# Kernel optimization log

Hardware: AMD Instinct MI355X
Metric: run time of the kernel (lower is better)

The kernel has to match this reference:

```python
import jax, jax.numpy as jnp
import numpy as np

V = 32000; D = 1024; L = 2; H = 16; KVH = 4; HD = D // H; E = 8; FF = 2048; K = 2
B = 2; S = 1024; WINDOW = 4096; THETA = 10000.0; EPS = 1e-6


def setup_inputs() -> dict:
    key = jax.random.key(0)
    ks = jax.random.split(key, 12)
    std = 0.02
    return {
        'tokens': jax.random.randint(ks[0], (B, S), 0, V),
        'tok_emb': jax.random.normal(ks[1], (V, D), jnp.float32),  # nn.Embedding default N(0,1)
        'norm1_w': jnp.ones((L, D), jnp.float32),
        'norm2_w': jnp.ones((L, D), jnp.float32),
        'wq': jax.random.normal(ks[2], (L, D, D), jnp.float32) * std,
        'wk': jax.random.normal(ks[3], (L, KVH * HD, D), jnp.float32) * std,
        'wv': jax.random.normal(ks[4], (L, KVH * HD, D), jnp.float32) * std,
        'wo': jax.random.normal(ks[5], (L, D, D), jnp.float32) * std,
        'router_w': jax.random.normal(ks[6], (L, E, D), jnp.float32) * (std / np.sqrt(D)),
        'w1': jax.random.normal(ks[7], (L, E, FF, D), jnp.float32) * std,
        'w2': jax.random.normal(ks[8], (L, E, FF, D), jnp.float32) * std,
        'w3': jax.random.normal(ks[9], (L, E, D, FF), jnp.float32) * std,
        'normf_w': jnp.ones((D,), jnp.float32),
        'head_w': jax.random.normal(ks[10], (V, D), jnp.float32) * std,
    }


def rmsnorm(x, w):
    # F.normalize(x, dim=-1, eps) * w * sqrt(d)
    n = jnp.linalg.norm(x, axis=-1, keepdims=True)
    return x / jnp.maximum(n, EPS) * w * np.float32(np.sqrt(x.shape[-1]))


def rope(x, cos, sin):
    # x: (b, s, h, hd); pairs are interleaved (even, odd) per view_as_complex
    x2 = x.reshape(x.shape[:-1] + (-1, 2))
    x0, x1 = x2[..., 0], x2[..., 1]
    o0 = x0 * cos - x1 * sin
    o1 = x0 * sin + x1 * cos
    return jnp.stack([o0, o1], axis=-1).reshape(x.shape)


def attention(x, wq, wk, wv, wo, cos, sin):
    b, s, _ = x.shape
    q = (x @ wq.T).reshape(b, s, H, HD)
    k = (x @ wk.T).reshape(b, s, KVH, HD)
    v = (x @ wv.T).reshape(b, s, KVH, HD)
    q = rope(q, cos, sin)
    k = rope(k, cos, sin)
    g = H // KVH
    k = jnp.repeat(k, g, axis=2)
    v = jnp.repeat(v, g, axis=2)
    scores = jnp.einsum('bqhd,bkhd->bhqk', q, k) / np.float32(np.sqrt(HD))
    i = jnp.arange(s)[:, None]; j = jnp.arange(s)[None, :]
    allow = (j <= i) & (i - j < WINDOW)  # causal + sliding window
    scores = jnp.where(allow, scores, -jnp.inf)
    attn = jax.nn.softmax(scores, axis=-1)
    out = jnp.einsum('bhqk,bkhd->bqhd', attn, v).reshape(b, s, D)
    return out @ wo.T


def moe(x, router_w, w1, w2, w3):
    b, s, d = x.shape
    logits = jnp.einsum('bsd,ed->bse', x, router_w)
    probs = jax.nn.softmax(logits, axis=-1)
    _, idx = jax.lax.top_k(probs, K)                      # (b, s, K)
    mask = jax.nn.one_hot(idx, E, dtype=x.dtype).sum(-2)  # (b, s, E) binary
    xt = x.reshape(-1, d)           # (T, d)
    mt = mask.reshape(-1, E)        # (T, E)
    # Dense masked dispatch: every expert computed on all tokens, combine masks to zero
    u = jnp.einsum('td,efd->etf', xt, w1)
    g = jax.nn.silu(u) * jnp.einsum('td,efd->etf', xt, w2)
    y = jnp.einsum('etf,edf->etd', g, w3)
    out = jnp.einsum('etd,te->td', y, mt).reshape(b, s, d)  # unweighted combine (per source)
    # aux losses
    z_loss = jnp.mean(jax.scipy.special.logsumexp(logits, axis=-1)) ** 2
    load = probs.sum(axis=0)  # (s, E), matching probs.sum(dim=0) in source
    load_loss = (jnp.std(load, ddof=1) / jnp.mean(load)) ** 2
    aux = 0.001 * z_loss + 0.001 * load_loss
    return out, aux


def _rope_tables(dtype):
    freqs = 1.0 / (THETA ** (np.arange(0, HD, 2, dtype=np.float32) / HD))
    ang = np.arange(S, dtype=np.float32)[:, None] * freqs[None, :]
    cos = jnp.asarray(np.cos(ang), dtype)[None, :, None, :]
    sin = jnp.asarray(np.sin(ang), dtype)[None, :, None, :]
    return cos, sin


def reference(tokens, tok_emb, norm1_w, norm2_w, wq, wk, wv, wo, router_w, w1, w2, w3, normf_w, head_w):
    x = tok_emb[tokens]  # (B, S, D)
    cos, sin = _rope_tables(x.dtype)
    attn_scale = np.float32(1.0 / np.sqrt(2.0 * L))
    aux_total = jnp.zeros((), x.dtype)
    for l in range(L):
        x = x + attn_scale * attention(rmsnorm(x, norm1_w[l]), wq[l], wk[l], wv[l], wo[l], cos, sin)
        mo, aux = moe(rmsnorm(x, norm2_w[l]), router_w[l], w1[l], w2[l], w3[l])
        x = x + mo
        aux_total = aux_total + aux
    logits = rmsnorm(x, normf_w) @ head_w.T
    return logits, aux_total
```

## Files before the change

kernel.cpp:

```cpp
#include <hip/hip_runtime.h>
#include <math.h>

#define DEV __device__ __forceinline__

using v8s = __attribute__((ext_vector_type(8))) short;
using v4f = __attribute__((ext_vector_type(4))) float;

DEV short f2bf(float f) {
    unsigned u = __float_as_uint(f);
    unsigned r = (u + 0x7fffu + ((u >> 16) & 1u)) >> 16;
    return (short)(unsigned short)r;
}
DEV float bf2f(short s) {
    return __uint_as_float(((unsigned)(unsigned short)s) << 16);
}

DEV void gload16(const short* g, short* l) {
    __builtin_amdgcn_global_load_lds((const __attribute__((address_space(1))) void*)g,
                                     (__attribute__((address_space(3))) void*)l,
                                     16, 0, 0);
}

DEV void raw_barrier() { asm volatile("s_barrier" ::: "memory"); }

DEV float block_sum256(float v, float* red) {
    __syncthreads();
#pragma unroll
    for (int o = 32; o >= 1; o >>= 1) v += __shfl_down(v, o, 64);
    if ((threadIdx.x & 63) == 0) red[threadIdx.x >> 6] = v;
    __syncthreads();
    return red[0] + red[1] + red[2] + red[3];
}
DEV float block_max256(float v, float* red) {
    __syncthreads();
#pragma unroll
    for (int o = 32; o >= 1; o >>= 1) v = fmaxf(v, __shfl_down(v, o, 64));
    if ((threadIdx.x & 63) == 0) red[threadIdx.x >> 6] = v;
    __syncthreads();
    return fmaxf(fmaxf(red[0], red[1]), fmaxf(red[2], red[3]));
}


__global__ __launch_bounds__(256) void conv_tile(const float* __restrict__ src,
                                                 short* __restrict__ hi, short* __restrict__ lo,
                                                 long nGroups, int Kg, long chunkRows, long chunkPanelStride) {
    const long panelElems = 128L * Kg * 8;
    for (long idx = (long)blockIdx.x * 256 + threadIdx.x; idx < nGroups; idx += (long)gridDim.x * 256) {
        long rrow = idx / Kg; int g = (int)(idx - rrow * Kg);
        long c = rrow / chunkRows; int ri = (int)(rrow - c * chunkRows);
        long panel = c * chunkPanelStride + (ri >> 7);
        long dst = panel * panelElems + ((long)(g >> 2) << 12) + ((long)(g & 3) << 10) + ((long)(ri & 127) << 3);
        const float4 f0 = ((const float4*)src)[idx * 2];
        const float4 f1 = ((const float4*)src)[idx * 2 + 1];
        short h0 = f2bf(f0.x), h1 = f2bf(f0.y), h2 = f2bf(f0.z), h3 = f2bf(f0.w);
        short h4 = f2bf(f1.x), h5 = f2bf(f1.y), h6 = f2bf(f1.z), h7 = f2bf(f1.w);
        *(ushort4*)(hi + dst)     = make_ushort4((unsigned short)h0, (unsigned short)h1,
                                                 (unsigned short)h2, (unsigned short)h3);
        *(ushort4*)(hi + dst + 4) = make_ushort4((unsigned short)h4, (unsigned short)h5,
                                                 (unsigned short)h6, (unsigned short)h7);
        if (lo) {
            short l0 = f2bf(f0.x - bf2f(h0)), l1 = f2bf(f0.y - bf2f(h1));
            short l2 = f2bf(f0.z - bf2f(h2)), l3 = f2bf(f0.w - bf2f(h3));
            short l4 = f2bf(f1.x - bf2f(h4)), l5 = f2bf(f1.y - bf2f(h5));
            short l6 = f2bf(f1.z - bf2f(h6)), l7 = f2bf(f1.w - bf2f(h7));
            *(ushort4*)(lo + dst)     = make_ushort4((unsigned short)l0, (unsigned short)l1,
                                                     (unsigned short)l2, (unsigned short)l3);
            *(ushort4*)(lo + dst + 4) = make_ushort4((unsigned short)l4, (unsigned short)l5,
                                                     (unsigned short)l6, (unsigned short)l7);
        }
    }
}

struct GemmP {
    const short* Ah; const short* Al;
    const short* Bh; const short* Bl;
    float* C; short* Ch; short* Cl;
    const int* cnt; const int* ppd; const int* lrow;
    long aPanelsZ;
    long strideAz;
    long strideBz, strideCz;
    int M, N, K, lda, ldc;
    float alpha;
    int outMode;
    int gqaB;
    int grouped;
    int causalSkip;
    int causalK;
    int ntiles, S, G;
};

template<bool SPLIT>
__global__ __launch_bounds__(256) void gemm_bt128(GemmP p) {
    const int lid = blockIdx.x;
    const int xcd = lid & 7, sI = lid >> 3;
    const int gi = xcd + 8 * (sI / p.S);
    if (gi >= p.G) return;
    const int mt = sI % p.S;
    const int nt = gi % p.ntiles;
    const int z  = gi / p.ntiles;
    if (p.causalSkip && nt > mt) return;

    const int tid = threadIdx.x;
    int Mz = p.grouped ? p.cnt[z] : p.M;
    if (mt * 128 >= Mz) return;

    long bOff;
    if (p.gqaB) { int b = z >> 4, h = z & 15; bOff = (long)(b * 4 + (h >> 2)) * p.strideBz; }
    else bOff = (long)z * p.strideBz;

    extern __shared__ short s0[];
    const int BUF = SPLIT ? 16384 : 8192;

    const int lane = tid & 63, w = tid >> 6;
    const int lr = lane & 15, lg = lane >> 4;
    const int wr = w >> 1, wc = w & 1;

    v4f acc[4][4];
#pragma unroll
    for (int i = 0; i < 4; ++i)
#pragma unroll
        for (int j = 0; j < 4; ++j) { acc[i][j][0] = 0.f; acc[i][j][1] = 0.f; acc[i][j][2] = 0.f; acc[i][j][3] = 0.f; }

    const short* bks  = p.Bh + bOff + (long)nt * 128 * p.K + (long)w * 1024 + lane * 8;
    const short* bksL = SPLIT ? p.Bl + bOff + (long)nt * 128 * p.K + (long)w * 1024 + lane * 8 : nullptr;

    long aPanel = (p.grouped ? (long)(p.ppd[z] >> 7) : (long)z * p.aPanelsZ) + mt;
    const short* aks  = p.Ah + aPanel * 128L * p.K + (long)w * 1024 + lane * 8;
    const short* aksL = SPLIT ? p.Al + aPanel * 128L * p.K + (long)w * 1024 + lane * 8 : nullptr;

    const int nIter = p.K >> 5;
    const int wb = w * 1024;
    {
        gload16(aks,       s0 + wb);
        gload16(aks + 512, s0 + wb + 512);
        gload16(bks,       s0 + 4096 + wb);
        gload16(bks + 512, s0 + 4096 + wb + 512);
        if (SPLIT) {
            gload16(aksL,       s0 + 8192 + wb);
            gload16(aksL + 512, s0 + 8192 + wb + 512);
            gload16(bksL,       s0 + 12288 + wb);
            gload16(bksL + 512, s0 + 12288 + wb + 512);
        }
    }
    for (int i = 0; i < nIter; ++i) {
        const int cur = i & 1;
        if (i + 1 < nIter) {
            raw_barrier();
            const long kb = (long)(i + 1) * 4096;
            short* base = s0 + (cur ^ 1) * BUF;
            gload16(aks + kb,       base + wb);
            gload16(aks + kb + 512, base + wb + 512);
            gload16(bks + kb,       base + 4096 + wb);
            gload16(bks + kb + 512, base + 4096 + wb + 512);
            if (SPLIT) {
                gload16(aksL + kb,       base + 8192 + wb);
                gload16(aksL + kb + 512, base + 8192 + wb + 512);
                gload16(bksL + kb,       base + 12288 + wb);
                gload16(bksL + kb + 512, base + 12288 + wb + 512);
            }
            if constexpr (SPLIT) asm volatile("s_waitcnt vmcnt(8)" ::: "memory");
            else                 asm volatile("s_waitcnt vmcnt(4)" ::: "memory");
        } else {
            asm volatile("s_waitcnt vmcnt(0)" ::: "memory");
        }
        raw_barrier();
        const short* base = s0 + cur * BUF;
        const int abase = lg * 1024 + (wr * 64 + lr) * 8;
        const int bbase = 4096 + lg * 1024 + (wc * 64 + lr) * 8;
        v8s ah[4], bh[4];
#pragma unroll
        for (int q = 0; q < 4; ++q) {
            ah[q] = *(const v8s*)(base + abase + q * 128);
            bh[q] = *(const v8s*)(base + bbase + q * 128);
        }
        if constexpr (SPLIT) {
            v8s al[4], bl[4];
#pragma unroll
            for (int q = 0; q < 4; ++q) {
                al[q] = *(const v8s*)(base + 8192 + abase + q * 128);
                bl[q] = *(const v8s*)(base + 8192 + bbase + q * 128);
            }
#pragma unroll
            for (int mi = 0; mi < 4; ++mi)
#pragma unroll
                for (int nj = 0; nj < 4; ++nj) {
                    acc[mi][nj] = __builtin_amdgcn_mfma_f32_16x16x32_bf16(ah[mi], bh[nj], acc[mi][nj], 0, 0, 0);
                    acc[mi][nj] = __builtin_amdgcn_mfma_f32_16x16x32_bf16(al[mi], bh[nj], acc[mi][nj], 0, 0, 0);
                    acc[mi][nj] = __builtin_amdgcn_mfma_f32_16x16x32_bf16(ah[mi], bl[nj], acc[mi][nj], 0, 0, 0);
                }
        } else {
#pragma unroll
            for (int mi = 0; mi < 4; ++mi)
#pragma unroll
                for (int nj = 0; nj < 4; ++nj)
                    acc[mi][nj] = __builtin_amdgcn_mfma_f32_16x16x32_bf16(ah[mi], bh[nj], acc[mi][nj], 0, 0, 0);
        }
    }

#pragma unroll
    for (int mi = 0; mi < 4; ++mi) {
        const int mrow = mt * 128 + wr * 64 + mi * 16 + lg * 4;
#pragma unroll
        for (int nj = 0; nj < 4; ++nj) {
            const int ncol = nt * 128 + wc * 64 + nj * 16 + lr;
            if (ncol < p.N) {
#pragma unroll
                for (int rr = 0; rr < 4; ++rr) {
                    const int m = mrow + rr;
                    if (m < Mz) {
                        float v = acc[mi][nj][rr] * p.alpha;
                        long crow;
                        if (p.grouped == 1)      crow = p.ppd[z] + m;
                        else if (p.grouped == 2) crow = p.lrow[z * 2048 + m];
                        else                     crow = m;
                        long co = (long)z * p.strideCz + crow * (long)p.ldc + ncol;
                        if (p.outMode == 0) p.C[co] = v;
                        else                p.C[co] += v;
                    }
                }
            }
        }
    }
}

template<bool SPLIT>
__global__ __launch_bounds__(512) void gemm_bt256(GemmP p) {
    const int lid = blockIdx.x;
    const int xcd = lid & 7, sI = lid >> 3;
    const int gi = xcd + 8 * (sI / p.S);
    if (gi >= p.G) return;
    const int mt = sI % p.S;
    const int nt = gi % p.ntiles;
    const int z  = gi / p.ntiles;
    if (p.causalSkip && nt > 2 * mt + 1) return;

    const int tid = threadIdx.x;
    int Mz = p.grouped ? p.cnt[z] : p.M;
    if (mt * 256 >= Mz) return;

    long bOff;
    if (p.gqaB) { int b = z >> 4, h = z & 15; bOff = (long)(b * 4 + (h >> 2)) * p.strideBz; }
    else bOff = (long)z * p.strideBz;

    extern __shared__ short s0[];
    const int BUF = SPLIT ? 24576 : 12288;

    const int lane = tid & 63, w = tid >> 6;
    const int lr = lane & 15, lg = lane >> 4;
    const int wr = w >> 1, wc = w & 1;

    v4f acc[4][4];
#pragma unroll
    for (int i = 0; i < 4; ++i)
#pragma unroll
        for (int j = 0; j < 4; ++j) { acc[i][j][0] = 0.f; acc[i][j][1] = 0.f; acc[i][j][2] = 0.f; acc[i][j][3] = 0.f; }

    const short* bks  = p.Bh + bOff + (long)nt * 128 * p.K + (long)w * 512 + lane * 8;
    const short* bksL = SPLIT ? p.Bl + bOff + (long)nt * 128 * p.K + (long)w * 512 + lane * 8 : nullptr;
    const long aPanelBase = (p.grouped ? (long)(p.ppd[z] >> 7) : (long)z * p.aPanelsZ) + 2L * mt;
    const int u0 = 2 * w, u1 = 2 * w + 1;
    const short* aks0  = p.Ah + (aPanelBase + (u0 >> 3)) * 128L * p.K + (long)(u0 & 7) * 512 + lane * 8;
    const short* aks1  = p.Ah + (aPanelBase + (u1 >> 3)) * 128L * p.K + (long)(u1 & 7) * 512 + lane * 8;
    const short* aks0L = SPLIT ? p.Al + (aPanelBase + (u0 >> 3)) * 128L * p.K + (long)(u0 & 7) * 512 + lane * 8 : nullptr;
    const short* aks1L = SPLIT ? p.Al + (aPanelBase + (u1 >> 3)) * 128L * p.K + (long)(u1 & 7) * 512 + lane * 8 : nullptr;
    short* dA0 = s0 + u0 * 512;
    short* dA1 = s0 + u1 * 512;
    short* dB  = s0 + 8192 + w * 512;

    const int nIter = p.K >> 5;
    {
        gload16(aks0, dA0);
        gload16(aks1, dA1);
        gload16(bks,  dB);
        if (SPLIT) {
            gload16(aks0L, dA0 + 12288);
            gload16(aks1L, dA1 + 12288);
            gload16(bksL,  dB + 12288);
        }
    }
    for (int i = 0; i < nIter; ++i) {
        const int cur = i & 1;
        if (i + 1 < nIter) {
            raw_barrier();
            const long kb = (long)(i + 1) * 4096;
            const int boff = (cur ^ 1) * BUF;
            gload16(aks0 + kb, dA0 + boff);
            gload16(aks1 + kb, dA1 + boff);
            gload16(bks + kb,  dB + boff);
            if (SPLIT) {
                gload16(aks0L + kb, dA0 + boff + 12288);
                gload16(aks1L + kb, dA1 + boff + 12288);
                gload16(bksL + kb,  dB + boff + 12288);
            }
            if constexpr (SPLIT) asm volatile("s_waitcnt vmcnt(6)" ::: "memory");
            else                 asm volatile("s_waitcnt vmcnt(3)" ::: "memory");
        } else {
            asm volatile("s_waitcnt vmcnt(0)" ::: "memory");
        }
        raw_barrier();
        const short* base = s0 + cur * BUF;
        const int abase = (wr >> 1) * 4096 + lg * 1024 + ((wr & 1) * 64 + lr) * 8;
        const int bbase = 8192 + lg * 1024 + (wc * 64 + lr) * 8;
        v8s ah[4], bh[4];
#pragma unroll
        for (int q = 0; q < 4; ++q) {
            ah[q] = *(const v8s*)(base + abase + q * 128);
            bh[q] = *(const v8s*)(base + bbase + q * 128);
        }
        if constexpr (SPLIT) {
            v8s al[4], bl[4];
#pragma unroll
            for (int q = 0; q < 4; ++q) {
                al[q] = *(const v8s*)(base + 12288 + abase + q * 128);
                bl[q] = *(const v8s*)(base + 12288 + bbase + q * 128);
            }
#pragma unroll
            for (int mi = 0; mi < 4; ++mi)
#pragma unroll
                for (int nj = 0; nj < 4; ++nj) {
                    acc[mi][nj] = __builtin_amdgcn_mfma_f32_16x16x32_bf16(ah[mi], bh[nj], acc[mi][nj], 0, 0, 0);
                    acc[mi][nj] = __builtin_amdgcn_mfma_f32_16x16x32_bf16(al[mi], bh[nj], acc[mi][nj], 0, 0, 0);
                    acc[mi][nj] = __builtin_amdgcn_mfma_f32_16x16x32_bf16(ah[mi], bl[nj], acc[mi][nj], 0, 0, 0);
                }
        } else {
#pragma unroll
            for (int mi = 0; mi < 4; ++mi)
#pragma unroll
                for (int nj = 0; nj < 4; ++nj)
                    acc[mi][nj] = __builtin_amdgcn_mfma_f32_16x16x32_bf16(ah[mi], bh[nj], acc[mi][nj], 0, 0, 0);
        }
    }

#pragma unroll
    for (int mi = 0; mi < 4; ++mi) {
        const int mrow = mt * 256 + wr * 64 + mi * 16 + lg * 4;
#pragma unroll
        for (int nj = 0; nj < 4; ++nj) {
            const int ncol = nt * 128 + wc * 64 + nj * 16 + lr;
            if (ncol < p.N) {
#pragma unroll
                for (int rr = 0; rr < 4; ++rr) {
                    const int m = mrow + rr;
                    if (m < Mz) {
                        float v = acc[mi][nj][rr] * p.alpha;
                        long crow;
                        if (p.grouped == 1)      crow = p.ppd[z] + m;
                        else if (p.grouped == 2) crow = p.lrow[z * 2048 + m];
                        else                     crow = m;
                        long co = (long)z * p.strideCz + crow * (long)p.ldc + ncol;
                        if (p.outMode == 0) p.C[co] = v;
                        else                p.C[co] += v;
                    }
                }
            }
        }
    }
}

__global__ __launch_bounds__(256) void gemm_pv(GemmP p) {
    const int lid = blockIdx.x;
    const int xcd = lid & 7, sI = lid >> 3;
    const int gi = xcd + 8 * (sI / p.S);
    if (gi >= p.G) return;
    const int mt = sI % p.S;
    const int z  = gi;
    const int tid = threadIdx.x;

    const int b = z >> 4, h = z & 15;
    const long bOff = (long)(b * 4 + (h >> 2)) * p.strideBz;

    extern __shared__ short s0[];
    short* Ahs = s0;
    short* Bhs = s0 + 4096;
    short* Als = s0 + 8192;
    short* Bls = s0 + 12288;

    const int lane = tid & 63, w = tid >> 6;
    const int lr = lane & 15, lg = lane >> 4;
    const int wr = w >> 1, wc = w & 1;

    v4f acc[4][4];
#pragma unroll
    for (int i = 0; i < 4; ++i)
#pragma unroll
        for (int j = 0; j < 4; ++j) { acc[i][j][0] = 0.f; acc[i][j][1] = 0.f; acc[i][j][2] = 0.f; acc[i][j][3] = 0.f; }

    const short* bks  = p.Bh + bOff + (long)w * 1024 + lane * 8;
    const short* bksL = p.Bl + bOff + (long)w * 1024 + lane * 8;

    const int r = tid & 127;
    const int kgA = tid >> 7;
    const int am = mt * 128 + r;
    const long arowoff = (long)z * p.strideAz + (long)am * p.lda;
    const short* aH = p.Ah + arowoff + kgA * 16;
    const short* aL = p.Al + arowoff + kgA * 16;
    short* sA0 = s0 + (kgA * 256 + r) * 8; short* sA1 = sA0 + 1024;
    short* sA0l = s0 + 8192 + (kgA * 256 + r) * 8; short* sA1l = sA0l + 1024;

    const int kEnd = min(p.K, (mt + 1) * 128);
    const int wb = w * 1024;
    for (int k0 = 0; k0 < kEnd; k0 += 32) {
        const long kb = (long)k0 * 128;
        uint4 a0 = *(const uint4*)(aH + k0);
        uint4 a1 = *(const uint4*)(aH + k0 + 8);
        uint4 a0l = *(const uint4*)(aL + k0);
        uint4 a1l = *(const uint4*)(aL + k0 + 8);
        __syncthreads();
        gload16(bks + kb,       Bhs + wb);
        gload16(bks + kb + 512, Bhs + wb + 512);
        gload16(bksL + kb,       Bls + wb);
        gload16(bksL + kb + 512, Bls + wb + 512);
        *(uint4*)sA0 = a0; *(uint4*)sA1 = a1;
        *(uint4*)sA0l = a0l; *(uint4*)sA1l = a1l;
        __syncthreads();
        const int abase = lg * 1024 + (wr * 64 + lr) * 8;
        const int bbase = lg * 1024 + (wc * 64 + lr) * 8;
        v8s ah[4], bh[4], al[4], bl[4];
#pragma unroll
        for (int q = 0; q < 4; ++q) {
            ah[q] = *(const v8s*)(Ahs + abase + q * 128);
            bh[q] = *(const v8s*)(Bhs + bbase + q * 128);
            al[q] = *(const v8s*)(Als + abase + q * 128);
            bl[q] = *(const v8s*)(Bls + bbase + q * 128);
        }
#pragma unroll
        for (int mi = 0; mi < 4; ++mi)
#pragma unroll
            for (int nj = 0; nj < 4; ++nj) {
                acc[mi][nj] = __builtin_amdgcn_mfma_f32_16x16x32_bf16(ah[mi], bh[nj], acc[mi][nj], 0, 0, 0);
                acc[mi][nj] = __builtin_amdgcn_mfma_f32_16x16x32_bf16(al[mi], bh[nj], acc[mi][nj], 0, 0, 0);
                acc[mi][nj] = __builtin_amdgcn_mfma_f32_16x16x32_bf16(ah[mi], bl[nj], acc[mi][nj], 0, 0, 0);
            }
    }

#pragma unroll
    for (int mi = 0; mi < 4; ++mi) {
        const int mrow = mt * 128 + wr * 64 + mi * 16 + lg * 4;
#pragma unroll
        for (int nj = 0; nj < 4; ++nj) {
            const int ncol = wc * 64 + nj * 16 + lr;
            if (ncol < 64) {
#pragma unroll
                for (int rr = 0; rr < 4; ++rr) {
                    const int m = mrow + rr;
                    float v = acc[mi][nj][rr];
                    int grow = b * 1024 + m, col = h * 64 + ncol;
                    long dst = ((long)(grow >> 7)) * 131072 + ((long)(col >> 5) << 12)
                             + ((long)((col >> 3) & 3) << 10) + ((long)(grow & 127) << 3) + (col & 7);
                    short hi = f2bf(v);
                    p.Ch[dst] = hi;
                    p.Cl[dst] = f2bf(v - bf2f(hi));
                }
            }
        }
    }
}

__global__ __launch_bounds__(256) void embed_kernel(const int* toks, const float* emb, float* X) {
    const int t = blockIdx.x;
    const int tok = toks[t];
    const float4* s = (const float4*)(emb + (size_t)tok * 1024);
    float4* d = (float4*)(X + (size_t)t * 1024);
    d[threadIdx.x] = s[threadIdx.x];
}

__global__ __launch_bounds__(256) void rmsnorm_split(const float* X, const float* w, short* oh, short* ol) {
    __shared__ float red[4];
    const long t = blockIdx.x;
    const float* r = X + t * 1024;
    float ss = 0.f;
    for (int j = threadIdx.x; j < 1024; j += 256) { float f = r[j]; ss += f * f; }
    ss = block_sum256(ss, red);
    const float sc = 32.f / fmaxf(sqrtf(ss), 1e-6f);
    if (threadIdx.x < 128) {
        const int g = threadIdx.x, f = g * 8;
        float v[8];
#pragma unroll
        for (int j = 0; j < 8; ++j) v[j] = r[f + j] * sc * w[f + j];
        long dst = (t >> 7) * 131072 + ((long)(g >> 2) << 12) + ((long)(g & 3) << 10) + ((t & 127) << 3);
        short h[8], lo[8];
#pragma unroll
        for (int j = 0; j < 8; ++j) { h[j] = f2bf(v[j]); lo[j] = f2bf(v[j] - bf2f(h[j])); }
        *(ushort4*)(oh + dst)     = make_ushort4((unsigned short)h[0], (unsigned short)h[1], (unsigned short)h[2], (unsigned short)h[3]);
        *(ushort4*)(oh + dst + 4) = make_ushort4((unsigned short)h[4], (unsigned short)h[5], (unsigned short)h[6], (unsigned short)h[7]);
        *(ushort4*)(ol + dst)     = make_ushort4((unsigned short)lo[0], (unsigned short)lo[1], (unsigned short)lo[2], (unsigned short)lo[3]);
        *(ushort4*)(ol + dst + 4) = make_ushort4((unsigned short)lo[4], (unsigned short)lo[5], (unsigned short)lo[6], (unsigned short)lo[7]);
    }
}

struct RopeF { float f[32]; };

__global__ __launch_bounds__(256) void rope_q_kernel(const float* QKV, short* OH, short* OL, RopeF rf) {
    const int idx = blockIdx.x * 256 + threadIdx.x;
    const int pp = idx & 31, h = (idx >> 5) & 15, s = (idx >> 9) & 1023, b = idx >> 19;
    const float* src = QKV + ((size_t)(b * 1024 + s)) * 1536 + h * 64 + 2 * pp;
    const float x0 = src[0], x1 = src[1];
    const float ang = (float)s * rf.f[pp];
    float sn, cs; sincosf(ang, &sn, &cs);
    const float o0 = x0 * cs - x1 * sn, o1 = x0 * sn + x1 * cs;
    const int z = b * 16 + h, d = 2 * pp;
    const long off = (long)z * 65536 + (long)(s >> 7) * 8192
                   + ((long)(d >> 5) << 12) + ((long)((d >> 3) & 3) << 10)
                   + ((long)(s & 127) << 3) + (d & 7);
    short h0 = f2bf(o0); OH[off] = h0; OL[off] = f2bf(o0 - bf2f(h0));
    short h1 = f2bf(o1); OH[off + 1] = h1; OL[off + 1] = f2bf(o1 - bf2f(h1));
}

__global__ __launch_bounds__(256) void rope_k_kernel(const float* QKV, short* KH, short* KL, RopeF rf) {
    const int idx = blockIdx.x * 256 + threadIdx.x;
    const int pp = idx & 31, kv = (idx >> 5) & 3, s = (idx >> 7) & 1023, b = idx >> 17;
    const float* src = QKV + ((size_t)(b * 1024 + s)) * 1536 + 1024 + kv * 64 + 2 * pp;
    const float x0 = src[0], x1 = src[1];
    const float ang = (float)s * rf.f[pp];
    float sn, cs; sincosf(ang, &sn, &cs);
    const float o0 = x0 * cs - x1 * sn, o1 = x0 * sn + x1 * cs;
    const int z = b * 4 + kv, d = 2 * pp;
    const long off = (long)z * 65536 + (long)(s >> 7) * 8192
                   + ((long)(d >> 5) << 12) + ((long)((d >> 3) & 3) << 10)
                   + ((long)(s & 127) << 3) + (d & 7);
    short h0 = f2bf(o0); KH[off] = h0; KL[off] = f2bf(o0 - bf2f(h0));
    short h1 = f2bf(o1); KH[off + 1] = h1; KL[off + 1] = f2bf(o1 - bf2f(h1));
}

__global__ __launch_bounds__(256) void transpose_v_kernel(const float* QKV, short* VH, short* VL) {
    const int idx = blockIdx.x * 256 + threadIdx.x;
    const int d = idx & 63, kv = (idx >> 6) & 3, s = (idx >> 8) & 1023, b = idx >> 18;
    const float f = QKV[((size_t)(b * 1024 + s)) * 1536 + 1280 + kv * 64 + d];
    const int z = b * 4 + kv;
    const long off = (long)z * 131072 + ((long)(s >> 5) << 12) + ((long)((s >> 3) & 3) << 10)
                   + ((long)d << 3) + (s & 7);
    short hi = f2bf(f);
    VH[off] = hi; VL[off] = f2bf(f - bf2f(hi));
    VH[off + 512] = 0; VL[off + 512] = 0;
}

__global__ __launch_bounds__(256) void attn_softmax(float* SC) {
    const long row = blockIdx.x;
    const int i = (int)(row & 1023);
    float* r = SC + row * 1024;
    __shared__ float buf[1024];
    __shared__ float red[4];
    const int n = i + 1;
    for (int j = threadIdx.x; j < n; j += 256) buf[j] = r[j];
    __syncthreads();
    float m = -INFINITY;
    for (int j = threadIdx.x; j < n; j += 256) m = fmaxf(m, buf[j]);
    m = block_max256(m, red);
    float s = 0.f;
    for (int j = threadIdx.x; j < n; j += 256) { float e = expf(buf[j] - m); buf[j] = e; s += e; }
    s = block_sum256(s, red);
    const float inv = 1.f / s;
    short* rh = (short*)r;
    short* rl = rh + 1024;
    __syncthreads();
    for (int j = threadIdx.x; j < 1024; j += 256) {
        float pv = (j < n) ? buf[j] * inv : 0.f;
        short hi = f2bf(pv);
        rh[j] = hi;
        rl[j] = f2bf(pv - bf2f(hi));
    }
}

__global__ __launch_bounds__(256) void router_kernel(const float* X, const float* wn, const float* rw,
                                                     float* probs, float* lse, int* cnt, int* ltok, int* lrow) {
    __shared__ float xs[1024];
    __shared__ float red[4];
    __shared__ float lg[8];
    const int t = blockIdx.x;
    const float* r = X + (size_t)t * 1024;
    for (int j = threadIdx.x; j < 1024; j += 256) xs[j] = r[j];
    __syncthreads();
    float ss = 0.f;
    for (int j = threadIdx.x; j < 1024; j += 256) ss += xs[j] * xs[j];
    ss = block_sum256(ss, red);
    const float sc = 32.f / fmaxf(sqrtf(ss), 1e-6f);
    float acc[8] = {0, 0, 0, 0, 0, 0, 0, 0};
    for (int j = threadIdx.x; j < 1024; j += 256) {
        const float xv = xs[j] * wn[j];
#pragma unroll
        for (int e = 0; e < 8; ++e) acc[e] += xv * rw[e * 1024 + j];
    }
#pragma unroll
    for (int e = 0; e < 8; ++e) {
        float s = block_sum256(acc[e], red);
        if (threadIdx.x == 0) lg[e] = s * sc;
    }
    __syncthreads();
    if (threadIdx.x == 0) {
        float m = lg[0];
        for (int e = 1; e < 8; ++e) m = fmaxf(m, lg[e]);
        float ex[8], se = 0.f;
        for (int e = 0; e < 8; ++e) { ex[e] = expf(lg[e] - m); se += ex[e]; }
        const float inv = 1.f / se;
        float pr[8];
        for (int e = 0; e < 8; ++e) { pr[e] = ex[e] * inv; probs[(size_t)t * 8 + e] = pr[e]; }
        lse[t] = m + logf(se);
        int i1 = 0;
        for (int e = 1; e < 8; ++e) if (pr[e] > pr[i1]) i1 = e;
        int i2 = (i1 == 0) ? 1 : 0;
        for (int e = 0; e < 8; ++e) if (e != i1 && pr[e] > pr[i2]) i2 = e;
        int s1 = atomicAdd(&cnt[i1], 1); ltok[i1 * 2048 + s1] = t; lrow[i1 * 2048 + s1] = 2 * t;
        int s2 = atomicAdd(&cnt[i2], 1); ltok[i2 * 2048 + s2] = t; lrow[i2 * 2048 + s2] = 2 * t + 1;
    }
}

__global__ void prefix_kernel(const int* cnt, int* ppd) {
    if (threadIdx.x == 0 && blockIdx.x == 0) {
        int a = 0;
        for (int e = 0; e < 8; ++e) { ppd[e] = a; a += ((cnt[e] + 255) >> 8) << 8; }
    }
}

__global__ __launch_bounds__(256) void gather_kernel(const short* XNH, const short* XNL,
                                                     const int* cnt, const int* ppd, const int* ltok,
                                                     short* GXNH, short* GXNL) {
    const int e = blockIdx.y, i = blockIdx.x;
    if (i >= cnt[e]) return;
    const int t = ltok[e * 2048 + i];
    const int pd = ppd[e] + i;
    const int plane = threadIdx.x >> 7, g = threadIdx.x & 127;
    const long goff = ((long)(g >> 2) << 12) + ((long)(g & 3) << 10);
    const long src = (long)(t >> 7) * 131072 + goff + ((t & 127) << 3);
    const long dst = (long)(pd >> 7) * 131072 + goff + ((pd & 127) << 3);
    const short* S = plane ? XNL : XNH;
    short* D = plane ? GXNL : GXNH;
    *(uint4*)(D + dst) = *(const uint4*)(S + src);
}

__global__ __launch_bounds__(256) void silu_mul(const float* U, short* HH, short* HL) {
    const int row = blockIdx.x, g = threadIdx.x;
    const float* ur = U + (long)row * 4096 + g * 8;
    const float4 u0 = *(const float4*)ur, u1 = *(const float4*)(ur + 4);
    const float4 g0 = *(const float4*)(ur + 2048), g1 = *(const float4*)(ur + 2052);
    float h[8];
    h[0] = (u0.x / (1.f + expf(-u0.x))) * g0.x;
    h[1] = (u0.y / (1.f + expf(-u0.y))) * g0.y;
    h[2] = (u0.z / (1.f + expf(-u0.z))) * g0.z;
    h[3] = (u0.w / (1.f + expf(-u0.w))) * g0.w;
    h[4] = (u1.x / (1.f + expf(-u1.x))) * g1.x;
    h[5] = (u1.y / (1.f + expf(-u1.y))) * g1.y;
    h[6] = (u1.z / (1.f + expf(-u1.z))) * g1.z;
    h[7] = (u1.w / (1.f + expf(-u1.w))) * g1.w;
    const long dst = (long)(row >> 7) * 262144 + ((long)(g >> 2) << 12) + ((long)(g & 3) << 10) + ((row & 127) << 3);
    short hh[8], ll[8];
#pragma unroll
    for (int j = 0; j < 8; ++j) { hh[j] = f2bf(h[j]); ll[j] = f2bf(h[j] - bf2f(hh[j])); }
    *(ushort4*)(HH + dst)     = make_ushort4((unsigned short)hh[0], (unsigned short)hh[1], (unsigned short)hh[2], (unsigned short)hh[3]);
    *(ushort4*)(HH + dst + 4) = make_ushort4((unsigned short)hh[4], (unsigned short)hh[5], (unsigned short)hh[6], (unsigned short)hh[7]);
    *(ushort4*)(HL + dst)     = make_ushort4((unsigned short)ll[0], (unsigned short)ll[1], (unsigned short)ll[2], (unsigned short)ll[3]);
    *(ushort4*)(HL + dst + 4) = make_ushort4((unsigned short)ll[4], (unsigned short)ll[5], (unsigned short)ll[6], (unsigned short)ll[7]);
}

__global__ __launch_bounds__(256) void combine_kernel(float* X, const float* Y) {
    const int i4 = blockIdx.x * 256 + threadIdx.x;
    const int t = i4 >> 8, d4 = i4 & 255;
    float4 x = ((float4*)X)[i4];
    const float4 a = ((const float4*)Y)[(size_t)(2 * t) * 256 + d4];
    const float4 b = ((const float4*)Y)[(size_t)(2 * t + 1) * 256 + d4];
    x.x += a.x + b.x; x.y += a.y + b.y; x.z += a.z + b.z; x.w += a.w + b.w;
    ((float4*)X)[i4] = x;
}

__global__ __launch_bounds__(256) void aux_kernel(const float* probs, const float* lse, float* auxb, int layer) {
    __shared__ float red[4];
    float sl = 0.f;
    for (int t = threadIdx.x; t < 2048; t += 256) sl += lse[t];
    sl = block_sum256(sl, red);
    float s1 = 0.f, s2 = 0.f;
    for (int i = threadIdx.x; i < 8192; i += 256) {
        const float l = probs[i] + probs[8192 + i];
        s1 += l; s2 += l * l;
    }
    s1 = block_sum256(s1, red);
    s2 = block_sum256(s2, red);
    if (threadIdx.x == 0) {
        const float ml = sl / 2048.f;
        const float mean = s1 / 8192.f;
        const float var = fmaxf((s2 - s1 * s1 / 8192.f) / 8191.f, 0.f);
        auxb[layer] = 0.001f * (ml * ml + var / (mean * mean));
    }
}

__global__ void finalize_aux(const float* auxb, float* out) {
    if (threadIdx.x == 0 && blockIdx.x == 0)
        out[(size_t)2 * 1024 * 32000] = auxb[0] + auxb[1];
}

static void run_gemm128(hipStream_t s, bool split, GemmP& p, int ntiles, int mtiles, int zdim) {
    p.ntiles = ntiles; p.S = mtiles;
    p.G = ntiles * zdim;
    int Gp = (p.G + 7) & ~7;
    long nb = (long)Gp * mtiles;
    dim3 g((unsigned)nb, 1, 1), b(256);
    if (split) gemm_bt128<true><<<g, b, 65536, s>>>(p);
    else       gemm_bt128<false><<<g, b, 32768, s>>>(p);
}

static void run_gemm256(hipStream_t s, bool split, GemmP& p, int ntiles, int mtiles, int zdim) {
    p.ntiles = ntiles; p.S = mtiles;
    p.G = ntiles * zdim;
    int Gp = (p.G + 7) & ~7;
    long nb = (long)Gp * mtiles;
    dim3 g((unsigned)nb, 1, 1), b(512);
    if (split) gemm_bt256<true><<<g, b, 98304, s>>>(p);
    else       gemm_bt256<false><<<g, b, 49152, s>>>(p);
}

static void run_tile(hipStream_t s, const float* src, short* hi, short* lo,
                     long rows, int K, long chunkRows, long chunkPanelStride) {
    long groups = rows * (K / 8);
    long nb = (groups + 255) / 256; if (nb > 2048) nb = 2048;
    conv_tile<<<(unsigned)nb, 256, 0, s>>>(src, hi, lo, groups, K / 8, chunkRows, chunkPanelStride);
}

extern "C" void kernel_launch(void* const* d_in, const int* in_sizes, int n_in,
                              void* d_out, int out_size, void* d_ws, size_t ws_size,
                              hipStream_t stream) {
    (void)in_sizes; (void)n_in; (void)out_size; (void)ws_size;
    const int*   tokens = (const int*)d_in[0];
    const float* tok_emb = (const float*)d_in[1];
    const float* norm1 = (const float*)d_in[2];
    const float* norm2 = (const float*)d_in[3];
    const float* wq = (const float*)d_in[4];
    const float* wk = (const float*)d_in[5];
    const float* wv = (const float*)d_in[6];
    const float* wo = (const float*)d_in[7];
    const float* rw = (const float*)d_in[8];
    const float* w1 = (const float*)d_in[9];
    const float* w2 = (const float*)d_in[10];
    const float* w3 = (const float*)d_in[11];
    const float* normf = (const float*)d_in[12];
    const float* headw = (const float*)d_in[13];
    float* out = (float*)d_out;

    char* w = (char*)d_ws;
    const size_t MB = 1024ull * 1024ull;
    float* X    = (float*)(w + 0);
    short* XNH  = (short*)(w + 8 * MB);
    short* XNL  = (short*)(w + 12 * MB);
    short* QRH  = (short*)(w + 16 * MB);
    short* QRL  = (short*)(w + 20 * MB);
    short* AOH  = QRH;
    short* AOL  = QRL;
    short* KRH  = (short*)(w + 24 * MB);
    short* KRL  = (short*)(w + 25 * MB);
    short* VTH  = (short*)(w + 26 * MB);
    short* VTL  = (short*)(w + 28 * MB);
    float* QKV  = (float*)(w + 32 * MB);
    float* SC   = (float*)(w + 32 * MB);
    short* GXNH = (short*)(w + 32 * MB);
    short* GXNL = (short*)(w + 44 * MB);
    float* U    = (float*)(w + 56 * MB);
    short* HH   = (short*)(w + 152 * MB);
    short* HL   = (short*)(w + 176 * MB);
    float* Y    = (float*)(w + 200 * MB);
    float* PROBS= (float*)(w + 216 * MB);
    float* LSE  = (float*)(w + 216 * MB + 65536);
    int*   CNT  = (int*)  (w + 216 * MB + 73728);
    int*   PPD  = (int*)  (w + 216 * MB + 73856);
    int*   LTOK = (int*)  (w + 216 * MB + 74240);
    int*   LROW = (int*)  (w + 216 * MB + 74240 + 65536);
    float* AUXB = (float*)(w + 216 * MB + 74240 + 131072);
    short* WQKVH = (short*)(w + 218 * MB);
    short* WQKVL = (short*)(w + 224 * MB);
    short* WOH   = (short*)(w + 230 * MB);
    short* WOL   = (short*)(w + 234 * MB);
    short* W12H  = (short*)(w + 238 * MB);
    short* W12L  = (short*)(w + 302 * MB);
    short* W3H   = (short*)(w + 366 * MB);
    short* W3L   = (short*)(w + 398 * MB);
    short* HDH   = (short*)(w + 302 * MB);

    RopeF rf;
    for (int i = 0; i < 32; ++i) {
        float t = (float)pow(10000.0, (double)(2 * i) / 64.0);
        rf.f[i] = 1.0f / t;
    }

    for (int l = 0; l < 2; ++l) {
        long qo = (long)l * 1572864;
        run_tile(stream, wq + (long)l * 1048576, WQKVH + qo,           WQKVL + qo,           1024, 1024, 1024, 8);
        run_tile(stream, wk + (long)l * 262144,  WQKVH + qo + 1048576, WQKVL + qo + 1048576, 256, 1024, 256, 2);
        run_tile(stream, wv + (long)l * 262144,  WQKVH + qo + 1310720, WQKVL + qo + 1310720, 256, 1024, 256, 2);
    }
    run_tile(stream, wo, WOH, WOL, 2048, 1024, 2048, 16);

    embed_kernel<<<2048, 256, 0, stream>>>(tokens, tok_emb, X);

    for (int l = 0; l < 2; ++l) {
        const bool msp = (l == 0);
        run_tile(stream, w1 + (long)l * 16777216, W12H,           msp ? W12L : nullptr,           16384, 1024, 2048, 32);
        run_tile(stream, w2 + (long)l * 16777216, W12H + 2097152, msp ? W12L + 2097152 : nullptr, 16384, 1024, 2048, 32);
        run_tile(stream, w3 + (long)l * 16777216, W3H,            msp ? W3L : nullptr,            8192, 2048, 8192, 64);

        rmsnorm_split<<<2048, 256, 0, stream>>>(X, norm1 + l * 1024, XNH, XNL);

        { GemmP p = {}; p.Ah = XNH; p.Al = XNL; p.Bh = WQKVH + (long)l * 1572864; p.Bl = WQKVL + (long)l * 1572864;
          p.C = QKV; p.M = 2048; p.N = 1536; p.K = 1024; p.aPanelsZ = 16; p.ldc = 1536; p.alpha = 1.f;
          run_gemm128(stream, true, p, 12, 16, 1); }

        rope_q_kernel<<<4096, 256, 0, stream>>>(QKV, QRH, QRL, rf);
        rope_k_kernel<<<1024, 256, 0, stream>>>(QKV, KRH, KRL, rf);
        transpose_v_kernel<<<2048, 256, 0, stream>>>(QKV, VTH, VTL);

        { GemmP p = {}; p.Ah = QRH; p.Al = QRL; p.Bh = KRH; p.Bl = KRL; p.C = SC;
          p.M = 1024; p.N = 1024; p.K = 64; p.aPanelsZ = 8; p.ldc = 1024;
          p.strideBz = 65536; p.strideCz = 1048576;
          p.alpha = 0.125f; p.gqaB = 1; p.causalSkip = 1;
          run_gemm256(stream, true, p, 8, 4, 32); }

        attn_softmax<<<32768, 256, 0, stream>>>(SC);

        { GemmP p = {}; p.Ah = (short*)SC; p.Al = (short*)SC + 1024; p.Bh = VTH; p.Bl = VTL; p.Ch = AOH; p.Cl = AOL;
          p.M = 1024; p.N = 64; p.K = 1024; p.lda = 2048;
          p.strideAz = 2097152; p.strideBz = 131072;
          p.ntiles = 1; p.S = 8; p.G = 32;
          long nb = 32L * 8;
          gemm_pv<<<dim3((unsigned)nb), dim3(256), 32768, stream>>>(p); }

        { GemmP p = {}; p.Ah = AOH; p.Al = AOL; p.Bh = WOH + (long)l * 1048576; p.Bl = WOL + (long)l * 1048576; p.C = X;
          p.M = 2048; p.N = 1024; p.K = 1024; p.aPanelsZ = 16; p.ldc = 1024;
          p.alpha = 0.5f; p.outMode = 1;
          run_gemm128(stream, true, p, 8, 16, 1); }

        rmsnorm_split<<<2048, 256, 0, stream>>>(X, norm2 + l * 1024, XNH, XNL);
        hipMemsetAsync(CNT, 0, 8 * sizeof(int), stream);
        router_kernel<<<2048, 256, 0, stream>>>(X, norm2 + l * 1024, rw + (size_t)l * 8 * 1024,
                                                PROBS, LSE, CNT, LTOK, LROW);
        prefix_kernel<<<1, 64, 0, stream>>>(CNT, PPD);
        { dim3 gg(2048, 8); gather_kernel<<<gg, 256, 0, stream>>>(XNH, XNL, CNT, PPD, LTOK, GXNH, GXNL); }

        { GemmP p = {}; p.Ah = GXNH; p.Al = GXNL; p.Bh = W12H; p.Bl = W12L; p.C = U;
          p.M = 2048; p.N = 4096; p.K = 1024; p.ldc = 4096;
          p.strideBz = 4194304; p.strideCz = 0; p.alpha = 1.f; p.grouped = 1;
          p.cnt = CNT; p.ppd = PPD; p.lrow = LROW;
          run_gemm256(stream, msp, p, 32, 8, 8); }
        silu_mul<<<6144, 256, 0, stream>>>(U, HH, HL);
        { GemmP p = {}; p.Ah = HH; p.Al = HL; p.Bh = W3H; p.Bl = W3L; p.C = Y;
          p.M = 2048; p.N = 1024; p.K = 2048; p.ldc = 1024;
          p.strideBz = 2097152; p.strideCz = 0; p.alpha = 1.f; p.grouped = 2;
          p.cnt = CNT; p.ppd = PPD; p.lrow = LROW;
          run_gemm256(stream, msp, p, 8, 8, 8); }
        combine_kernel<<<2048, 256, 0, stream>>>(X, Y);
        aux_kernel<<<1, 256, 0, stream>>>(PROBS, LSE, AUXB, l);

        if (l == 0)
            run_tile(stream, headw, HDH, nullptr, 32000, 1024, 32000, 250);
    }

    rmsnorm_split<<<2048, 256, 0, stream>>>(X, normf, XNH, XNL);
    { GemmP p = {}; p.Ah = XNH; p.Bh = HDH; p.C = out;
      p.M = 2048; p.N = 32000; p.K = 1024; p.aPanelsZ = 16; p.ldc = 32000; p.alpha = 1.f;
      run_gemm256(stream, false, p, 250, 8, 1); }
    finalize_aux<<<1, 1, 0, stream>>>(AUXB, out);
}
```

Before: 2.164 ms.

## Reorder GEMM block mapping, fuse rope/transpose kernels, use 128-tile grouped MoE GEMMs

Changes the block-index decode in the GEMM kernels so that consecutive launch slots iterate over the n/z group dimension before the m tile. This alters which tiles run concurrently and how operands are shared in cache. Merges the three rope/transpose launches into one kernel dispatched by block id, removing two launches. In split-precision mode the grouped MoE GEMMs now use 128-row tiles instead of 256, giving more, smaller blocks and less waste on experts with few rows, at the cost of more B-matrix reloads.

```diff
diff --git a/kernel.cpp b/kernel.cpp
--- a/kernel.cpp
+++ b/kernel.cpp
@@ -85,17 +85,17 @@
     int gqaB;
     int grouped;
     int causalSkip;
-    int causalK;
-    int ntiles, S, G;
+    int ntiles, G, Gx;
 };
 
 template<bool SPLIT>
 __global__ __launch_bounds__(256) void gemm_bt128(GemmP p) {
     const int lid = blockIdx.x;
     const int xcd = lid & 7, sI = lid >> 3;
-    const int gi = xcd + 8 * (sI / p.S);
+    const int gx = sI % p.Gx;
+    const int mt = sI / p.Gx;
+    const int gi = xcd + 8 * gx;
     if (gi >= p.G) return;
-    const int mt = sI % p.S;
     const int nt = gi % p.ntiles;
     const int z  = gi / p.ntiles;
     if (p.causalSkip && nt > mt) return;
@@ -227,9 +227,10 @@
 __global__ __launch_bounds__(512) void gemm_bt256(GemmP p) {
     const int lid = blockIdx.x;
     const int xcd = lid & 7, sI = lid >> 3;
-    const int gi = xcd + 8 * (sI / p.S);
+    const int gx = sI % p.Gx;
+    const int mt = sI / p.Gx;
+    const int gi = xcd + 8 * gx;
     if (gi >= p.G) return;
-    const int mt = sI % p.S;
     const int nt = gi % p.ntiles;
     const int z  = gi / p.ntiles;
     if (p.causalSkip && nt > 2 * mt + 1) return;
@@ -360,10 +361,9 @@
 __global__ __launch_bounds__(256) void gemm_pv(GemmP p) {
     const int lid = blockIdx.x;
     const int xcd = lid & 7, sI = lid >> 3;
-    const int gi = xcd + 8 * (sI / p.S);
-    if (gi >= p.G) return;
-    const int mt = sI % p.S;
-    const int z  = gi;
+    const int gx = sI % 4;
+    const int mt = sI / 4;
+    const int z = xcd + 8 * gx;
     const int tid = threadIdx.x;
 
     const int b = z >> 4, h = z & 15;
@@ -490,48 +490,50 @@
 
 struct RopeF { float f[32]; };
 
-__global__ __launch_bounds__(256) void rope_q_kernel(const float* QKV, short* OH, short* OL, RopeF rf) {
-    const int idx = blockIdx.x * 256 + threadIdx.x;
-    const int pp = idx & 31, h = (idx >> 5) & 15, s = (idx >> 9) & 1023, b = idx >> 19;
-    const float* src = QKV + ((size_t)(b * 1024 + s)) * 1536 + h * 64 + 2 * pp;
-    const float x0 = src[0], x1 = src[1];
-    const float ang = (float)s * rf.f[pp];
-    float sn, cs; sincosf(ang, &sn, &cs);
-    const float o0 = x0 * cs - x1 * sn, o1 = x0 * sn + x1 * cs;
-    const int z = b * 16 + h, d = 2 * pp;
-    const long off = (long)z * 65536 + (long)(s >> 7) * 8192
-                   + ((long)(d >> 5) << 12) + ((long)((d >> 3) & 3) << 10)
-                   + ((long)(s & 127) << 3) + (d & 7);
-    short h0 = f2bf(o0); OH[off] = h0; OL[off] = f2bf(o0 - bf2f(h0));
-    short h1 = f2bf(o1); OH[off + 1] = h1; OL[off + 1] = f2bf(o1 - bf2f(h1));
-}
-
-__global__ __launch_bounds__(256) void rope_k_kernel(const float* QKV, short* KH, short* KL, RopeF rf) {
-    const int idx = blockIdx.x * 256 + threadIdx.x;
-    const int pp = idx & 31, kv = (idx >> 5) & 3, s = (idx >> 7) & 1023, b = idx >> 17;
-    const float* src = QKV + ((size_t)(b * 1024 + s)) * 1536 + 1024 + kv * 64 + 2 * pp;
-    const float x0 = src[0], x1 = src[1];
-    const float ang = (float)s * rf.f[pp];
-    float sn, cs; sincosf(ang, &sn, &cs);
-    const float o0 = x0 * cs - x1 * sn, o1 = x0 * sn + x1 * cs;
-    const int z = b * 4 + kv, d = 2 * pp;
-    const long off = (long)z * 65536 + (long)(s >> 7) * 8192
-                   + ((long)(d >> 5) << 12) + ((long)((d >> 3) & 3) << 10)
-                   + ((long)(s & 127) << 3) + (d & 7);
-    short h0 = f2bf(o0); KH[off] = h0; KL[off] = f2bf(o0 - bf2f(h0));
-    short h1 = f2bf(o1); KH[off + 1] = h1; KL[off + 1] = f2bf(o1 - bf2f(h1));
-}
-
-__global__ __launch_bounds__(256) void transpose_v_kernel(const float* QKV, short* VH, short* VL) {
-    const int idx = blockIdx.x * 256 + threadIdx.x;
-    const int d = idx & 63, kv = (idx >> 6) & 3, s = (idx >> 8) & 1023, b = idx >> 18;
-    const float f = QKV[((size_t)(b * 1024 + s)) * 1536 + 1280 + kv * 64 + d];
-    const int z = b * 4 + kv;
-    const long off = (long)z * 131072 + ((long)(s >> 5) << 12) + ((long)((s >> 3) & 3) << 10)
-                   + ((long)d << 3) + (s & 7);
-    short hi = f2bf(f);
-    VH[off] = hi; VL[off] = f2bf(f - bf2f(hi));
-    VH[off + 512] = 0; VL[off + 512] = 0;
+__global__ __launch_bounds__(256) void rope_fused_kernel(const float* QKV,
+                                                         short* QH, short* QL,
+                                                         short* KH, short* KL,
+                                                         short* VH, short* VL, RopeF rf) {
+    const int bid = blockIdx.x;
+    if (bid < 4096) {
+        const int idx = bid * 256 + threadIdx.x;
+        const int pp = idx & 31, h = (idx >> 5) & 15, s = (idx >> 9) & 1023, b = idx >> 19;
+        const float* src = QKV + ((size_t)(b * 1024 + s)) * 1536 + h * 64 + 2 * pp;
+        const float x0 = src[0], x1 = src[1];
+        const float ang = (float)s * rf.f[pp];
+        float sn, cs; sincosf(ang, &sn, &cs);
+        const float o0 = x0 * cs - x1 * sn, o1 = x0 * sn + x1 * cs;
+        const int z = b * 16 + h, d = 2 * pp;
+        const long off = (long)z * 65536 + (long)(s >> 7) * 8192
+                       + ((long)(d >> 5) << 12) + ((long)((d >> 3) & 3) << 10)
+                       + ((long)(s & 127) << 3) + (d & 7);
+        short h0 = f2bf(o0); QH[off] = h0; QL[off] = f2bf(o0 - bf2f(h0));
+        short h1 = f2bf(o1); QH[off + 1] = h1; QL[off + 1] = f2bf(o1 - bf2f(h1));
+    } else if (bid < 5120) {
+        const int idx = (bid - 4096) * 256 + threadIdx.x;
+        const int pp = idx & 31, kv = (idx >> 5) & 3, s = (idx >> 7) & 1023, b = idx >> 17;
+        const float* src = QKV + ((size_t)(b * 1024 + s)) * 1536 + 1024 + kv * 64 + 2 * pp;
+        const float x0 = src[0], x1 = src[1];
+        const float ang = (float)s * rf.f[pp];
+        float sn, cs; sincosf(ang, &sn, &cs);
+        const float o0 = x0 * cs - x1 * sn, o1 = x0 * sn + x1 * cs;
+        const int z = b * 4 + kv, d = 2 * pp;
+        const long off = (long)z * 65536 + (long)(s >> 7) * 8192
+                       + ((long)(d >> 5) << 12) + ((long)((d >> 3) & 3) << 10)
+                       + ((long)(s & 127) << 3) + (d & 7);
+        short h0 = f2bf(o0); KH[off] = h0; KL[off] = f2bf(o0 - bf2f(h0));
+        short h1 = f2bf(o1); KH[off + 1] = h1; KL[off + 1] = f2bf(o1 - bf2f(h1));
+    } else {
+        const int idx = (bid - 5120) * 256 + threadIdx.x;
+        const int d = idx & 63, kv = (idx >> 6) & 3, s = (idx >> 8) & 1023, b = idx >> 18;
+        const float f = QKV[((size_t)(b * 1024 + s)) * 1536 + 1280 + kv * 64 + d];
+        const int z = b * 4 + kv;
+        const long off = (long)z * 131072 + ((long)(s >> 5) << 12) + ((long)((s >> 3) & 3) << 10)
+                       + ((long)d << 3) + (s & 7);
+        short hi = f2bf(f);
+        VH[off] = hi; VL[off] = f2bf(f - bf2f(hi));
+        VH[off + 512] = 0; VL[off + 512] = 0;
+    }
 }
 
 __global__ __launch_bounds__(256) void attn_softmax(float* SC) {
@@ -687,20 +689,20 @@
 }
 
 static void run_gemm128(hipStream_t s, bool split, GemmP& p, int ntiles, int mtiles, int zdim) {
-    p.ntiles = ntiles; p.S = mtiles;
+    p.ntiles = ntiles;
     p.G = ntiles * zdim;
-    int Gp = (p.G + 7) & ~7;
-    long nb = (long)Gp * mtiles;
+    p.Gx = (p.G + 7) >> 3;
+    long nb = 8L * p.Gx * mtiles;
     dim3 g((unsigned)nb, 1, 1), b(256);
     if (split) gemm_bt128<true><<<g, b, 65536, s>>>(p);
     else       gemm_bt128<false><<<g, b, 32768, s>>>(p);
 }
 
 static void run_gemm256(hipStream_t s, bool split, GemmP& p, int ntiles, int mtiles, int zdim) {
-    p.ntiles = ntiles; p.S = mtiles;
+    p.ntiles = ntiles;
     p.G = ntiles * zdim;
-    int Gp = (p.G + 7) & ~7;
-    long nb = (long)Gp * mtiles;
+    p.Gx = (p.G + 7) >> 3;
+    long nb = 8L * p.Gx * mtiles;
     dim3 g((unsigned)nb, 1, 1), b(512);
     if (split) gemm_bt256<true><<<g, b, 98304, s>>>(p);
     else       gemm_bt256<false><<<g, b, 49152, s>>>(p);
@@ -799,9 +801,7 @@
           p.C = QKV; p.M = 2048; p.N = 1536; p.K = 1024; p.aPanelsZ = 16; p.ldc = 1536; p.alpha = 1.f;
           run_gemm128(stream, true, p, 12, 16, 1); }
 
-        rope_q_kernel<<<4096, 256, 0, stream>>>(QKV, QRH, QRL, rf);
-        rope_k_kernel<<<1024, 256, 0, stream>>>(QKV, KRH, KRL, rf);
-        transpose_v_kernel<<<2048, 256, 0, stream>>>(QKV, VTH, VTL);
+        rope_fused_kernel<<<7168, 256, 0, stream>>>(QKV, QRH, QRL, KRH, KRL, VTH, VTL, rf);
 
         { GemmP p = {}; p.Ah = QRH; p.Al = QRL; p.Bh = KRH; p.Bl = KRL; p.C = SC;
           p.M = 1024; p.N = 1024; p.K = 64; p.aPanelsZ = 8; p.ldc = 1024;
@@ -814,9 +814,7 @@
         { GemmP p = {}; p.Ah = (short*)SC; p.Al = (short*)SC + 1024; p.Bh = VTH; p.Bl = VTL; p.Ch = AOH; p.Cl = AOL;
           p.M = 1024; p.N = 64; p.K = 1024; p.lda = 2048;
           p.strideAz = 2097152; p.strideBz = 131072;
-          p.ntiles = 1; p.S = 8; p.G = 32;
-          long nb = 32L * 8;
-          gemm_pv<<<dim3((unsigned)nb), dim3(256), 32768, stream>>>(p); }
+          gemm_pv<<<dim3(256), dim3(256), 32768, stream>>>(p); }
 
         { GemmP p = {}; p.Ah = AOH; p.Al = AOL; p.Bh = WOH + (long)l * 1048576; p.Bl = WOL + (long)l * 1048576; p.C = X;
           p.M = 2048; p.N = 1024; p.K = 1024; p.aPanelsZ = 16; p.ldc = 1024;
@@ -830,17 +828,33 @@
         prefix_kernel<<<1, 64, 0, stream>>>(CNT, PPD);
         { dim3 gg(2048, 8); gather_kernel<<<gg, 256, 0, stream>>>(XNH, XNL, CNT, PPD, LTOK, GXNH, GXNL); }
 
-        { GemmP p = {}; p.Ah = GXNH; p.Al = GXNL; p.Bh = W12H; p.Bl = W12L; p.C = U;
-          p.M = 2048; p.N = 4096; p.K = 1024; p.ldc = 4096;
-          p.strideBz = 4194304; p.strideCz = 0; p.alpha = 1.f; p.grouped = 1;
-          p.cnt = CNT; p.ppd = PPD; p.lrow = LROW;
-          run_gemm256(stream, msp, p, 32, 8, 8); }
+        if (msp) {
+            GemmP p = {}; p.Ah = GXNH; p.Al = GXNL; p.Bh = W12H; p.Bl = W12L; p.C = U;
+            p.M = 2048; p.N = 4096; p.K = 1024; p.ldc = 4096;
+            p.strideBz = 4194304; p.strideCz = 0; p.alpha = 1.f; p.grouped = 1;
+            p.cnt = CNT; p.ppd = PPD; p.lrow = LROW;
+            run_gemm128(stream, true, p, 32, 16, 8);
+        } else {
+            GemmP p = {}; p.Ah = GXNH; p.Al = GXNL; p.Bh = W12H; p.Bl = W12L; p.C = U;
+            p.M = 2048; p.N = 4096; p.K = 1024; p.ldc = 4096;
+            p.strideBz = 4194304; p.strideCz = 0; p.alpha = 1.f; p.grouped = 1;
+            p.cnt = CNT; p.ppd = PPD; p.lrow = LROW;
+            run_gemm256(stream, false, p, 32, 8, 8);
+        }
         silu_mul<<<6144, 256, 0, stream>>>(U, HH, HL);
-        { GemmP p = {}; p.Ah = HH; p.Al = HL; p.Bh = W3H; p.Bl = W3L; p.C = Y;
-          p.M = 2048; p.N = 1024; p.K = 2048; p.ldc = 1024;
-          p.strideBz = 2097152; p.strideCz = 0; p.alpha = 1.f; p.grouped = 2;
-          p.cnt = CNT; p.ppd = PPD; p.lrow = LROW;
-          run_gemm256(stream, msp, p, 8, 8, 8); }
+        if (msp) {
+            GemmP p = {}; p.Ah = HH; p.Al = HL; p.Bh = W3H; p.Bl = W3L; p.C = Y;
+            p.M = 2048; p.N = 1024; p.K = 2048; p.ldc = 1024;
+            p.strideBz = 2097152; p.strideCz = 0; p.alpha = 1.f; p.grouped = 2;
+            p.cnt = CNT; p.ppd = PPD; p.lrow = LROW;
+            run_gemm128(stream, true, p, 8, 16, 8);
+        } else {
+            GemmP p = {}; p.Ah = HH; p.Al = HL; p.Bh = W3H; p.Bl = W3L; p.C = Y;
+            p.M = 2048; p.N = 1024; p.K = 2048; p.ldc = 1024;
+            p.strideBz = 2097152; p.strideCz = 0; p.alpha = 1.f; p.grouped = 2;
+            p.cnt = CNT; p.ppd = PPD; p.lrow = LROW;
+            run_gemm256(stream, false, p, 8, 8, 8);
+        }
         combine_kernel<<<2048, 256, 0, stream>>>(X, Y);
         aux_kernel<<<1, 256, 0, stream>>>(PROBS, LSE, AUXB, l);
 
```

After: 2.020 ms. -6.6%, faster.
